# Kernel tuning notes

Hardware: AMD Instinct MI355X
Metric: run time of the kernel (lower is better)

Reference implementation:

```python
import jax, jax.numpy as jnp
import numpy as np

STEPS = 12

def setup_inputs() -> dict:
    key = jax.random.key(0)
    ks = jax.random.split(key, 5)
    B, T, F, C, NEG = 16, 2048, 512, 256, 10
    true_latent = jax.random.normal(ks[0], (B, T, F), jnp.float32)
    context_latent = jax.random.normal(ks[1], (B, T, C), jnp.float32)
    Wl = jax.random.normal(ks[2], (F, C), jnp.float32) * (1.0 / np.sqrt(F))
    bl = jnp.zeros((C,), jnp.float32)
    Ws = jax.random.normal(ks[3], (STEPS,), jnp.float32)
    bs = jnp.zeros((STEPS,), jnp.float32)
    # negative-sample timestep indices: uniform in [0, T-1), shifted +1 when >= t so idx != t
    raw = jax.random.randint(ks[4], (B, NEG, T), 0, T - 1)
    t_idx = jnp.arange(T)[None, None, :]
    neg_indices = jnp.where(raw >= t_idx, raw + 1, raw).astype(jnp.int32)
    return {"true_latent": true_latent, "context_latent": context_latent,
            "Wl": Wl, "bl": bl, "Ws": Ws, "bs": bs, "neg_indices": neg_indices}

def reference(true_latent, context_latent, Wl, bl, Ws, bs, neg_indices):
    B, T, _ = true_latent.shape
    # project_latent: Conv1D(C, k=1) == per-timestep linear
    tl = true_latent @ Wl + bl                         # [B, T, C]
    # project_steps: Conv2DTranspose(steps, k=1) on [B,T,C,1] == scalar 1->steps linear
    preds = context_latent[..., None] * Ws + bs        # [B, T, C, S]
    # gather negatives within each sample: negs[b, n, t, :] = tl[b, neg_indices[b, n, t], :]
    negs = jnp.take_along_axis(tl[:, None, :, :], neg_indices[..., None], axis=2)  # [B, NEG, T, C]
    targets = jnp.concatenate([tl[None], jnp.transpose(negs, (1, 0, 2, 3))], axis=0)  # [copies, B, T, C]
    copies = targets.shape[0]
    chunks = []
    for i in range(STEPS):  # small fixed loop over prediction steps
        lg = jnp.einsum('stf,cstf->tsc', preds[:, :T - i, :, i], targets[:, :, i:, :])
        chunks.append(lg.reshape(-1))
    logits = jnp.concatenate(chunks, 0).reshape(-1, copies)
    # CategoricalCrossentropy(from_logits=True, SUM) with one-hot label at column 0
    loss = jnp.sum(jax.nn.logsumexp(logits, axis=-1) - logits[:, 0])
    return loss.reshape(1)
```

## Files before the change

### kernel.cpp

```cpp
#include <hip/hip_runtime.h>
#include <math.h>

#define BB 16
#define TT 2048
#define FF 512
#define CC 256
#define NEG 10
#define NSTEPS 12
#define COPIES 11
#define MM (BB * TT)

__global__ __launch_bounds__(256) void proj_gemm_kernel(
    const float* __restrict__ A,
    const float* __restrict__ W,
    const float* __restrict__ bias,
    float* __restrict__ Out) {
  __shared__ __align__(16) float As[16][132];
  __shared__ __align__(16) float Bs[16][128];
  const int tid = threadIdx.x;
  const int bm = blockIdx.x * 128;
  const int bn = blockIdx.y * 128;
  const int tx = tid & 15;
  const int ty = tid >> 4;
  const int am = tid >> 1;
  const int ak = (tid & 1) * 8;
  const int bk = tid >> 5;
  const int bc = (tid & 31) * 4;
  float acc[8][8] = {};

  const float* Ap = &A[(size_t)(bm + am) * FF + ak];
  const float* Bp = &W[(size_t)bk * CC + bn + bc];
  float4 pa0 = *reinterpret_cast<const float4*>(Ap);
  float4 pa1 = *reinterpret_cast<const float4*>(Ap + 4);
  float4 pb0 = *reinterpret_cast<const float4*>(Bp);
  float4 pb1 = *reinterpret_cast<const float4*>(Bp + 8 * CC);

  for (int kt = 0; kt < FF / 16; ++kt) {
    __syncthreads();
    As[ak + 0][am] = pa0.x; As[ak + 1][am] = pa0.y;
    As[ak + 2][am] = pa0.z; As[ak + 3][am] = pa0.w;
    As[ak + 4][am] = pa1.x; As[ak + 5][am] = pa1.y;
    As[ak + 6][am] = pa1.z; As[ak + 7][am] = pa1.w;
    *reinterpret_cast<float4*>(&Bs[bk][bc]) = pb0;
    *reinterpret_cast<float4*>(&Bs[bk + 8][bc]) = pb1;
    __syncthreads();
    if (kt + 1 < FF / 16) {
      const float* Apn = Ap + (kt + 1) * 16;
      const float* Bpn = Bp + (size_t)(kt + 1) * 16 * CC;
      pa0 = *reinterpret_cast<const float4*>(Apn);
      pa1 = *reinterpret_cast<const float4*>(Apn + 4);
      pb0 = *reinterpret_cast<const float4*>(Bpn);
      pb1 = *reinterpret_cast<const float4*>(Bpn + 8 * CC);
    }
#pragma unroll
    for (int kk = 0; kk < 16; ++kk) {
      const float4 a0 = *reinterpret_cast<const float4*>(&As[kk][ty * 8]);
      const float4 a1 = *reinterpret_cast<const float4*>(&As[kk][ty * 8 + 4]);
      const float4 b0 = *reinterpret_cast<const float4*>(&Bs[kk][tx * 8]);
      const float4 b1 = *reinterpret_cast<const float4*>(&Bs[kk][tx * 8 + 4]);
      const float av[8] = {a0.x, a0.y, a0.z, a0.w, a1.x, a1.y, a1.z, a1.w};
      const float bv[8] = {b0.x, b0.y, b0.z, b0.w, b1.x, b1.y, b1.z, b1.w};
#pragma unroll
      for (int i = 0; i < 8; ++i)
#pragma unroll
        for (int j = 0; j < 8; ++j) acc[i][j] = fmaf(av[i], bv[j], acc[i][j]);
    }
  }
  float bz[8];
#pragma unroll
  for (int j = 0; j < 8; ++j) bz[j] = bias[bn + tx * 8 + j];
#pragma unroll
  for (int i = 0; i < 8; ++i) {
    float4 o0, o1;
    o0.x = acc[i][0] + bz[0]; o0.y = acc[i][1] + bz[1];
    o0.z = acc[i][2] + bz[2]; o0.w = acc[i][3] + bz[3];
    o1.x = acc[i][4] + bz[4]; o1.y = acc[i][5] + bz[5];
    o1.z = acc[i][6] + bz[6]; o1.w = acc[i][7] + bz[7];
    float* orow = &Out[(size_t)(bm + ty * 8 + i) * CC + bn + tx * 8];
    *reinterpret_cast<float4*>(orow) = o0;
    *reinterpret_cast<float4*>(orow + 4) = o1;
  }
}

#define TP 16
#define NROWS (TP + COPIES)
#define NCP 3
__global__ __launch_bounds__(256, 4) void cpc_loss_kernel(
    const float* __restrict__ ctx,
    const float* __restrict__ tl,
    const int* __restrict__ negs,
    const float* __restrict__ Ws,
    const float* __restrict__ bs,
    float* __restrict__ partials) {
  __shared__ __align__(16) float lds[NROWS * CC];
  const int tid = threadIdx.x;
  const int tloc = tid >> 4;
  const int ch = (tid >> 2) & 3;
  const int kg = tid & 3;
  const int wg = blockIdx.x;
  const int b = (wg & 7) | (((wg >> 3) & 1) << 3);
  const int chunk = wg >> 4;
  const int tp0 = chunk * TP;
  const int tp = tp0 + tloc;

  for (int idx = tid; idx < NROWS * (CC / 4); idx += 256) {
    const int r = idx >> 6;
    const int c4 = idx & 63;
    const int t = tp0 - COPIES + r;
    float4 v = make_float4(0.f, 0.f, 0.f, 0.f);
    if (t >= 0) v = *reinterpret_cast<const float4*>(&ctx[((size_t)b * TT + t) * CC + c4 * 4]);
    *reinterpret_cast<float4*>(&lds[r * CC + ((c4 ^ (r & 7)) << 2)]) = v;
  }

  unsigned off[NCP];
#pragma unroll
  for (int j = 0; j < NCP; ++j) {
    int cp = ch * 3 + j;
    if (cp > 10) cp = 10;
    const int u = (cp == 0) ? tp : negs[((size_t)b * NEG + (cp - 1)) * TT + tp];
    off[j] = (unsigned)(((size_t)b * TT + u) * CC) * 4u;
  }
  const char* tlb = (const char*)tl;

  int rowb[NSTEPS], rsw[NSTEPS];
#pragma unroll
  for (int i = 0; i < NSTEPS; ++i) {
    const int r = tloc + COPIES - i;
    rowb[i] = r * CC;
    rsw[i] = r & 7;
  }

  float acc[NSTEPS][NCP] = {};
  float tsum[NCP] = {};
  __syncthreads();

  float4 tg[NCP];
#pragma unroll
  for (int j = 0; j < NCP; ++j)
    tg[j] = *reinterpret_cast<const float4*>(tlb + off[j] + (unsigned)(kg << 4));
#pragma unroll
  for (int c4 = 0; c4 < 16; ++c4) {
    float4 tgn[NCP];
    if (c4 < 15) {
      const unsigned e4n = (unsigned)((((c4 + 1) << 2) | kg) << 4);
#pragma unroll
      for (int j = 0; j < NCP; ++j)
        tgn[j] = *reinterpret_cast<const float4*>(tlb + off[j] + e4n);
    }
#pragma unroll
    for (int j = 0; j < NCP; ++j)
      tsum[j] += (tg[j].x + tg[j].y) + (tg[j].z + tg[j].w);
    const int e4 = (c4 << 2) | kg;
#pragma unroll
    for (int i = 0; i < NSTEPS; ++i) {
      const float4 cx = *reinterpret_cast<const float4*>(&lds[rowb[i] + ((e4 ^ rsw[i]) << 2)]);
#pragma unroll
      for (int j = 0; j < NCP; ++j) {
        acc[i][j] = fmaf(cx.x, tg[j].x, acc[i][j]);
        acc[i][j] = fmaf(cx.y, tg[j].y, acc[i][j]);
        acc[i][j] = fmaf(cx.z, tg[j].z, acc[i][j]);
        acc[i][j] = fmaf(cx.w, tg[j].w, acc[i][j]);
      }
    }
    if (c4 < 15) {
#pragma unroll
      for (int j = 0; j < NCP; ++j) tg[j] = tgn[j];
    }
  }

#pragma unroll
  for (int i = 0; i < NSTEPS; ++i)
#pragma unroll
    for (int j = 0; j < NCP; ++j) {
      acc[i][j] += __shfl_xor(acc[i][j], 1);
      acc[i][j] += __shfl_xor(acc[i][j], 2);
    }
#pragma unroll
  for (int j = 0; j < NCP; ++j) {
    tsum[j] += __shfl_xor(tsum[j], 1);
    tsum[j] += __shfl_xor(tsum[j], 2);
  }

  __syncthreads();
  float* sd = lds;
  float* ts = lds + TP * NSTEPS * 13;
  if (kg == 0) {
#pragma unroll
    for (int j = 0; j < NCP; ++j) {
      const int cp = ch * 3 + j;
      if (cp <= 10) {
        ts[tloc * 13 + cp] = tsum[j];
#pragma unroll
        for (int i = 0; i < NSTEPS; ++i) sd[(tloc * NSTEPS + i) * 13 + cp] = acc[i][j];
      }
    }
  }
  __syncthreads();

  float contrib = 0.f;
  if (tid < TP * NSTEPS) {
    const int tt = tid / NSTEPS;
    const int i = tid - tt * NSTEPS;
    if (i <= tp0 + tt) {
      const float w = Ws[i], bbias = bs[i];
      const float* drow = &sd[tid * 13];
      const float* trow = &ts[tt * 13];
      float lg[COPIES];
      float m = -INFINITY;
#pragma unroll
      for (int cp = 0; cp < COPIES; ++cp) {
        lg[cp] = fmaf(w, drow[cp], bbias * trow[cp]);
        m = fmaxf(m, lg[cp]);
      }
      float s = 0.f;
#pragma unroll
      for (int cp = 0; cp < COPIES; ++cp) s += expf(lg[cp] - m);
      contrib = m + logf(s) - lg[0];
    }
  }

  __syncthreads();
  lds[tid] = contrib;
  __syncthreads();
  for (int s = 128; s > 0; s >>= 1) {
    if (tid < s) lds[tid] += lds[tid + s];
    __syncthreads();
  }
  if (tid == 0) partials[wg] = lds[0];
}

#define NBLK (BB * (TT / TP))
__global__ __launch_bounds__(256) void reduce_kernel(const float* __restrict__ partials,
                                                     float* __restrict__ out) {
  __shared__ double sred[256];
  double acc = 0.0;
  for (int idx = threadIdx.x; idx < NBLK; idx += 256) acc += (double)partials[idx];
  sred[threadIdx.x] = acc;
  __syncthreads();
  for (int s = 128; s > 0; s >>= 1) {
    if (threadIdx.x < s) sred[threadIdx.x] += sred[threadIdx.x + s];
    __syncthreads();
  }
  if (threadIdx.x == 0) out[0] = (float)sred[0];
}

extern "C" void kernel_launch(void* const* d_in, const int* in_sizes, int n_in,
                              void* d_out, int out_size, void* d_ws, size_t ws_size,
                              hipStream_t stream) {
  const float* true_latent = (const float*)d_in[0];
  const float* context_latent = (const float*)d_in[1];
  const float* Wl = (const float*)d_in[2];
  const float* bl = (const float*)d_in[3];
  const float* Ws = (const float*)d_in[4];
  const float* bs = (const float*)d_in[5];
  const int* negs = (const int*)d_in[6];

  float* tl = (float*)d_ws;
  float* partials = (float*)((char*)d_ws + (size_t)MM * CC * sizeof(float));

  dim3 g1(MM / 128, CC / 128);
  proj_gemm_kernel<<<g1, 256, 0, stream>>>(true_latent, Wl, bl, tl);
  cpc_loss_kernel<<<NBLK, 256, 0, stream>>>(context_latent, tl, negs, Ws, bs, partials);
  reduce_kernel<<<1, 256, 0, stream>>>(partials, (float*)d_out);
}
```

Measured before the change: 273.0 us.

## Retile projection GEMM to 128x64 with double-buffered LDS and strided fragments

Changes the projection GEMM tile from 128x128 to 128x64 so each thread accumulates 8x4 instead of 8x8. The shared-memory tiles are now double-buffered, which drops one barrier per k-step, and the launch bound is set to 4 blocks per CU. Threads read A fragments at stride 64 rather than as contiguous 8-row chunks, which changes the LDS access pattern. The grid doubles, giving more occupancy and more blocks, at the cost of less register reuse and twice as many reloads of A across the N dimension.

```diff
diff --git a/kernel.cpp b/kernel.cpp
--- a/kernel.cpp
+++ b/kernel.cpp
@@ -10,76 +10,90 @@
 #define COPIES 11
 #define MM (BB * TT)
 
-__global__ __launch_bounds__(256) void proj_gemm_kernel(
+#define GA_STRIDE 132
+#define GB_STRIDE 68
+__global__ __launch_bounds__(256, 4) void proj_gemm_kernel(
     const float* __restrict__ A,
     const float* __restrict__ W,
     const float* __restrict__ bias,
     float* __restrict__ Out) {
-  __shared__ __align__(16) float As[16][132];
-  __shared__ __align__(16) float Bs[16][128];
+  __shared__ __align__(16) float As[2][16 * GA_STRIDE];
+  __shared__ __align__(16) float Bs[2][16 * GB_STRIDE];
   const int tid = threadIdx.x;
   const int bm = blockIdx.x * 128;
-  const int bn = blockIdx.y * 128;
+  const int bn = blockIdx.y * 64;
   const int tx = tid & 15;
   const int ty = tid >> 4;
   const int am = tid >> 1;
   const int ak = (tid & 1) * 8;
-  const int bk = tid >> 5;
-  const int bc = (tid & 31) * 4;
-  float acc[8][8] = {};
+  const int brow = tid >> 4;
+  const int bc4 = tid & 15;
+  float acc[8][4] = {};
 
   const float* Ap = &A[(size_t)(bm + am) * FF + ak];
-  const float* Bp = &W[(size_t)bk * CC + bn + bc];
+  const float* Bp = &W[(size_t)brow * CC + bn + bc4 * 4];
+
   float4 pa0 = *reinterpret_cast<const float4*>(Ap);
   float4 pa1 = *reinterpret_cast<const float4*>(Ap + 4);
   float4 pb0 = *reinterpret_cast<const float4*>(Bp);
-  float4 pb1 = *reinterpret_cast<const float4*>(Bp + 8 * CC);
-
-  for (int kt = 0; kt < FF / 16; ++kt) {
-    __syncthreads();
-    As[ak + 0][am] = pa0.x; As[ak + 1][am] = pa0.y;
-    As[ak + 2][am] = pa0.z; As[ak + 3][am] = pa0.w;
-    As[ak + 4][am] = pa1.x; As[ak + 5][am] = pa1.y;
-    As[ak + 6][am] = pa1.z; As[ak + 7][am] = pa1.w;
-    *reinterpret_cast<float4*>(&Bs[bk][bc]) = pb0;
-    *reinterpret_cast<float4*>(&Bs[bk + 8][bc]) = pb1;
-    __syncthreads();
-    if (kt + 1 < FF / 16) {
+  {
+    float* a = As[0];
+    a[(ak + 0) * GA_STRIDE + am] = pa0.x; a[(ak + 1) * GA_STRIDE + am] = pa0.y;
+    a[(ak + 2) * GA_STRIDE + am] = pa0.z; a[(ak + 3) * GA_STRIDE + am] = pa0.w;
+    a[(ak + 4) * GA_STRIDE + am] = pa1.x; a[(ak + 5) * GA_STRIDE + am] = pa1.y;
+    a[(ak + 6) * GA_STRIDE + am] = pa1.z; a[(ak + 7) * GA_STRIDE + am] = pa1.w;
+    *reinterpret_cast<float4*>(&Bs[0][brow * GB_STRIDE + bc4 * 4]) = pb0;
+  }
+  __syncthreads();
+
+  const int NT = FF / 16;
+  for (int kt = 0; kt < NT; ++kt) {
+    const int cur = kt & 1;
+    if (kt + 1 < NT) {
       const float* Apn = Ap + (kt + 1) * 16;
       const float* Bpn = Bp + (size_t)(kt + 1) * 16 * CC;
       pa0 = *reinterpret_cast<const float4*>(Apn);
       pa1 = *reinterpret_cast<const float4*>(Apn + 4);
       pb0 = *reinterpret_cast<const float4*>(Bpn);
-      pb1 = *reinterpret_cast<const float4*>(Bpn + 8 * CC);
-    }
+    }
+    const float* a = As[cur];
+    const float* bsh = Bs[cur];
 #pragma unroll
     for (int kk = 0; kk < 16; ++kk) {
-      const float4 a0 = *reinterpret_cast<const float4*>(&As[kk][ty * 8]);
-      const float4 a1 = *reinterpret_cast<const float4*>(&As[kk][ty * 8 + 4]);
-      const float4 b0 = *reinterpret_cast<const float4*>(&Bs[kk][tx * 8]);
-      const float4 b1 = *reinterpret_cast<const float4*>(&Bs[kk][tx * 8 + 4]);
+      const float4 a0 = *reinterpret_cast<const float4*>(&a[kk * GA_STRIDE + ty * 4]);
+      const float4 a1 = *reinterpret_cast<const float4*>(&a[kk * GA_STRIDE + 64 + ty * 4]);
+      const float4 b0 = *reinterpret_cast<const float4*>(&bsh[kk * GB_STRIDE + tx * 4]);
       const float av[8] = {a0.x, a0.y, a0.z, a0.w, a1.x, a1.y, a1.z, a1.w};
-      const float bv[8] = {b0.x, b0.y, b0.z, b0.w, b1.x, b1.y, b1.z, b1.w};
+      const float bv[4] = {b0.x, b0.y, b0.z, b0.w};
 #pragma unroll
       for (int i = 0; i < 8; ++i)
 #pragma unroll
-        for (int j = 0; j < 8; ++j) acc[i][j] = fmaf(av[i], bv[j], acc[i][j]);
-    }
-  }
-  float bz[8];
-#pragma unroll
-  for (int j = 0; j < 8; ++j) bz[j] = bias[bn + tx * 8 + j];
-#pragma unroll
-  for (int i = 0; i < 8; ++i) {
-    float4 o0, o1;
-    o0.x = acc[i][0] + bz[0]; o0.y = acc[i][1] + bz[1];
-    o0.z = acc[i][2] + bz[2]; o0.w = acc[i][3] + bz[3];
-    o1.x = acc[i][4] + bz[4]; o1.y = acc[i][5] + bz[5];
-    o1.z = acc[i][6] + bz[6]; o1.w = acc[i][7] + bz[7];
-    float* orow = &Out[(size_t)(bm + ty * 8 + i) * CC + bn + tx * 8];
-    *reinterpret_cast<float4*>(orow) = o0;
-    *reinterpret_cast<float4*>(orow + 4) = o1;
-  }
+        for (int j = 0; j < 4; ++j) acc[i][j] = fmaf(av[i], bv[j], acc[i][j]);
+    }
+    if (kt + 1 < NT) {
+      float* an = As[cur ^ 1];
+      an[(ak + 0) * GA_STRIDE + am] = pa0.x; an[(ak + 1) * GA_STRIDE + am] = pa0.y;
+      an[(ak + 2) * GA_STRIDE + am] = pa0.z; an[(ak + 3) * GA_STRIDE + am] = pa0.w;
+      an[(ak + 4) * GA_STRIDE + am] = pa1.x; an[(ak + 5) * GA_STRIDE + am] = pa1.y;
+      an[(ak + 6) * GA_STRIDE + am] = pa1.z; an[(ak + 7) * GA_STRIDE + am] = pa1.w;
+      *reinterpret_cast<float4*>(&Bs[cur ^ 1][brow * GB_STRIDE + bc4 * 4]) = pb0;
+      __syncthreads();
+    }
+  }
+
+  const float4 b4 = *reinterpret_cast<const float4*>(&bias[bn + tx * 4]);
+  const float bz[4] = {b4.x, b4.y, b4.z, b4.w};
+#pragma unroll
+  for (int h = 0; h < 2; ++h)
+#pragma unroll
+    for (int i = 0; i < 4; ++i) {
+      float4 o;
+      o.x = acc[h * 4 + i][0] + bz[0];
+      o.y = acc[h * 4 + i][1] + bz[1];
+      o.z = acc[h * 4 + i][2] + bz[2];
+      o.w = acc[h * 4 + i][3] + bz[3];
+      *reinterpret_cast<float4*>(&Out[(size_t)(bm + h * 64 + ty * 4 + i) * CC + bn + tx * 4]) = o;
+    }
 }
 
 #define TP 16
@@ -258,7 +272,7 @@
   float* tl = (float*)d_ws;
   float* partials = (float*)((char*)d_ws + (size_t)MM * CC * sizeof(float));
 
-  dim3 g1(MM / 128, CC / 128);
+  dim3 g1(MM / 128, CC / 64);
   proj_gemm_kernel<<<g1, 256, 0, stream>>>(true_latent, Wl, bl, tl);
   cpc_loss_kernel<<<NBLK, 256, 0, stream>>>(context_latent, tl, negs, Ws, bs, partials);
   reduce_kernel<<<1, 256, 0, stream>>>(partials, (float*)d_out);
```

New measurement: 264.2 us. -3.2%, faster.
